# Performance work log

Measured on AMD Instinct MI355X. Metric: run time of the kernel, lower is better.

Reference implementation:

```python
import jax, jax.numpy as jnp
import numpy as np

D_MODEL = 1024
N_HEADS = 16
N_KV_HEADS = 4
HEAD_DIM = D_MODEL // N_HEADS
GROUP = N_HEADS // N_KV_HEADS
ROPE_BASE = 10000.0


def _rope(x):
    # x: (B, H, T, Dh); standard rotate-half RoPE, base 10000
    B, H, T, Dh = x.shape
    inv_freq = 1.0 / (ROPE_BASE ** (jnp.arange(0, Dh, 2, dtype=jnp.float32) / Dh))
    t = jnp.arange(T, dtype=jnp.float32)
    freqs = t[:, None] * inv_freq[None, :]              # (T, Dh/2)
    emb = jnp.concatenate([freqs, freqs], axis=-1)      # (T, Dh)
    cos = jnp.cos(emb)[None, None].astype(x.dtype)
    sin = jnp.sin(emb)[None, None].astype(x.dtype)
    x1, x2 = x[..., : Dh // 2], x[..., Dh // 2 :]
    rot = jnp.concatenate([-x2, x1], axis=-1)
    return x * cos + rot * sin


def setup_inputs() -> dict:
    key = jax.random.key(0)
    ks = jax.random.split(key, 5)
    B, T = 2, 2048
    s = 1.0 / np.sqrt(D_MODEL)
    return {
        "x": jax.random.normal(ks[0], (B, T, D_MODEL), dtype=jnp.float32),
        "wq": jax.random.normal(ks[1], (D_MODEL, N_HEADS * HEAD_DIM), dtype=jnp.float32) * s,
        "wk": jax.random.normal(ks[2], (D_MODEL, N_KV_HEADS * HEAD_DIM), dtype=jnp.float32) * s,
        "wv": jax.random.normal(ks[3], (D_MODEL, N_KV_HEADS * HEAD_DIM), dtype=jnp.float32) * s,
        "wo": jax.random.normal(ks[4], (N_HEADS * HEAD_DIM, D_MODEL), dtype=jnp.float32) * s,
    }


def reference(x, wq, wk, wv, wo):
    B, T, _ = x.shape
    q = (x @ wq).reshape(B, T, N_HEADS, HEAD_DIM).transpose(0, 2, 1, 3)      # (B,H,T,Dh)
    k = (x @ wk).reshape(B, T, N_KV_HEADS, HEAD_DIM).transpose(0, 2, 1, 3)   # (B,Hk,T,Dh)
    v = (x @ wv).reshape(B, T, N_KV_HEADS, HEAD_DIM).transpose(0, 2, 1, 3)
    q = _rope(q)
    k = _rope(k)
    # repeat_interleave kv heads group_size times -> (B, H, T, Dh)
    k = jnp.repeat(k, GROUP, axis=1)
    v = jnp.repeat(v, GROUP, axis=1)
    scale = 1.0 / np.sqrt(HEAD_DIM)
    scores = jnp.einsum("bhqd,bhkd->bhqk", q, k) * scale                      # (B,H,T,T)
    causal = jnp.tril(jnp.ones((T, T), dtype=bool))
    scores = jnp.where(causal[None, None], scores, -jnp.inf)
    attn = jax.nn.softmax(scores, axis=-1)
    out = jnp.einsum("bhqk,bhkd->bhqd", attn, v)                              # (B,H,T,Dh)
    out = out.transpose(0, 2, 1, 3).reshape(B, T, N_HEADS * HEAD_DIM)
    return out @ wo
```

## Files before the change

kernel.cpp:

```cpp
#include <hip/hip_runtime.h>

typedef short bshort8 __attribute__((ext_vector_type(8)));
typedef float f32x4 __attribute__((ext_vector_type(4)));

#define DEVFN static __device__ __forceinline__

DEVFN unsigned short f2bf(float f) {
    union { float f; unsigned u; } v; v.f = f;
    unsigned r = (v.u + 0x7FFFu + ((v.u >> 16) & 1u)) >> 16;
    return (unsigned short)r;
}

DEVFN float bf2f(unsigned short u) {
    union { unsigned u; float f; } v; v.u = (unsigned)u << 16;
    return v.f;
}

DEVFN unsigned cvt_pk_bf16(float a, float b) {
    unsigned r;
    asm("v_cvt_pk_bf16_f32 %0, %1, %2" : "=v"(r) : "v"(a), "v"(b));
    return r;
}

DEVFN float exp2_fast(float x) {
    float r;
    asm("v_exp_f32 %0, %1" : "=v"(r) : "v"(x));
    return r;
}

DEVFN float max3f(float a, float b, float c) {
    float r;
    asm("v_max3_f32 %0, %1, %2, %3" : "=v"(r) : "v"(a), "v"(b), "v"(c));
    return r;
}

DEVFN int swzf(int row) { return (row & 7) ^ ((row >> 3) & 7); }
DEVFN int swzf2(int row) { return (row & 3) ^ ((row >> 2) & 3); }

#define GLDS16(g, l)                                                            \
    __builtin_amdgcn_global_load_lds(                                           \
        (__attribute__((address_space(1))) void*)(g),                           \
        (__attribute__((address_space(3))) void*)(l), 16, 0, 0)

__global__ void prep_kernel(const float* __restrict__ x,
                            const float* __restrict__ wq,
                            const float* __restrict__ wk,
                            const float* __restrict__ wv,
                            const float* __restrict__ wo,
                            unsigned short* __restrict__ xb,
                            unsigned short* __restrict__ wt,
                            unsigned short* __restrict__ wot,
                            float2* __restrict__ cs) {
    const int z = blockIdx.z;
    int tx = threadIdx.x, ty = threadIdx.y;
    if (z >= 5) {
        int i = ((z - 5) * 1024 + blockIdx.y * 32 + blockIdx.x) * 256 + ty * 32 + tx;
        float4 v = ((const float4*)x)[i];
        ushort4 o;
        o.x = f2bf(v.x); o.y = f2bf(v.y); o.z = f2bf(v.z); o.w = f2bf(v.w);
        ((ushort4*)xb)[i] = o;
        return;
    }
    if (z == 4) {
        int idx = (blockIdx.y * 32 + blockIdx.x) * 256 + ty * 32 + tx;
        if (idx < 65536) {
            int t = idx >> 5, i = idx & 31;
            float inv_freq = powf(10000.0f, -(float)i / 32.0f);
            float a = (float)t * inv_freq;
            cs[idx] = make_float2(cosf(a), sinf(a));
        }
        return;
    }
    const float* src;
    unsigned short* dst;
    int N;
    if (z == 0)      { src = wq; dst = wt;                N = 1024; }
    else if (z == 1) { src = wk; dst = wt + 1024 * 1024;  N = 256; }
    else if (z == 2) { src = wv; dst = wt + 1280 * 1024;  N = 256; }
    else             { src = wo; dst = wot;               N = 1024; }
    if (blockIdx.x * 32 >= N) return;
    __shared__ float tile[32][33];
    int n0 = blockIdx.x * 32, k0 = blockIdx.y * 32;
#pragma unroll
    for (int i = 0; i < 4; i++)
        tile[ty + i * 8][tx] = src[(size_t)(k0 + ty + i * 8) * N + n0 + tx];
    __syncthreads();
#pragma unroll
    for (int i = 0; i < 4; i++)
        dst[(size_t)(n0 + ty + i * 8) * 1024 + k0 + tx] = f2bf(tile[tx][ty + i * 8]);
}


__global__ __launch_bounds__(256) void gemm_qkv_kernel(
    const unsigned short* __restrict__ xb, const unsigned short* __restrict__ wt,
    const float2* __restrict__ cs, unsigned short* __restrict__ Qb,
    unsigned short* __restrict__ Kb, unsigned short* __restrict__ Vt) {
    __shared__ char smem[49152];
    const int tid = threadIdx.x;
    const int lane = tid & 63, w = tid >> 6;
    const int m0 = blockIdx.y * 128, n0 = blockIdx.x * 64;
    const int l15 = lane & 15, g = lane >> 4;
    const int l8 = lane >> 3, c8 = lane & 7;

    const unsigned short* srcA[4];
    int dstA[4];
#pragma unroll
    for (int j = 0; j < 4; j++) {
        int row = w * 32 + j * 8 + l8;
        srcA[j] = xb + (size_t)(m0 + row) * 1024 + (c8 ^ swzf(row)) * 8;
        dstA[j] = w * 4096 + j * 1024 + lane * 16;
    }
    const unsigned short* srcB[2];
    int dstB[2];
#pragma unroll
    for (int j = 0; j < 2; j++) {
        int row = w * 16 + j * 8 + l8;
        srcB[j] = wt + (size_t)(n0 + row) * 1024 + (c8 ^ swzf(row)) * 8;
        dstB[j] = 0x8000 + w * 2048 + j * 1024 + lane * 16;
    }

    int aOff[2][2], bOff[4][2];
#pragma unroll
    for (int fm = 0; fm < 2; fm++) {
        int row = w * 32 + fm * 16 + l15;
#pragma unroll
        for (int ks = 0; ks < 2; ks++)
            aOff[fm][ks] = row * 128 + (((ks * 4 + g) ^ swzf(row)) << 4);
    }
#pragma unroll
    for (int fn = 0; fn < 4; fn++) {
        int row = fn * 16 + l15;
#pragma unroll
        for (int ks = 0; ks < 2; ks++)
            bOff[fn][ks] = row * 128 + (((ks * 4 + g) ^ swzf(row)) << 4);
    }

    f32x4 acc[2][4] = {};
#pragma unroll
    for (int j = 0; j < 4; j++) GLDS16(srcA[j], smem + dstA[j]);
#pragma unroll
    for (int j = 0; j < 2; j++) GLDS16(srcB[j], smem + dstB[j]);
    asm volatile("s_waitcnt vmcnt(0)" ::: "memory");
    __builtin_amdgcn_s_barrier();

    for (int kt = 0; kt < 16; kt++) {
        const int curA = (kt & 1) << 14;
        const int curB = (kt & 1) << 13;
        if (kt < 15) {
            const int nA = curA ^ 0x4000, nB = curB ^ 0x2000;
#pragma unroll
            for (int j = 0; j < 4; j++)
                GLDS16(srcA[j] + (kt + 1) * 64, smem + nA + dstA[j]);
#pragma unroll
            for (int j = 0; j < 2; j++)
                GLDS16(srcB[j] + (kt + 1) * 64, smem + nB + dstB[j]);
        }
        bshort8 af[2][2], bf[4][2];
#pragma unroll
        for (int fm = 0; fm < 2; fm++)
#pragma unroll
            for (int ks = 0; ks < 2; ks++)
                af[fm][ks] = *(const bshort8*)(smem + curA + aOff[fm][ks]);
#pragma unroll
        for (int fn = 0; fn < 4; fn++)
#pragma unroll
            for (int ks = 0; ks < 2; ks++)
                bf[fn][ks] = *(const bshort8*)(smem + 0x8000 + curB + bOff[fn][ks]);
        asm volatile("s_waitcnt lgkmcnt(0)" ::: "memory");
        __builtin_amdgcn_sched_barrier(0);
#pragma unroll
        for (int fm = 0; fm < 2; fm++)
#pragma unroll
            for (int fn = 0; fn < 4; fn++) {
                acc[fm][fn] = __builtin_amdgcn_mfma_f32_16x16x32_bf16(
                    af[fm][0], bf[fn][0], acc[fm][fn], 0, 0, 0);
                acc[fm][fn] = __builtin_amdgcn_mfma_f32_16x16x32_bf16(
                    af[fm][1], bf[fn][1], acc[fm][fn], 0, 0, 0);
            }
        if (kt < 15) {
            asm volatile("s_waitcnt vmcnt(0)" ::: "memory");
            __builtin_amdgcn_s_barrier();
        }
    }

    const bool isV = (n0 >= 1280);
    const bool isK = (n0 >= 1024) && !isV;
#pragma unroll
    for (int fm = 0; fm < 2; fm++) {
#pragma unroll
        for (int r = 0; r < 4; r++) {
            int m = m0 + w * 32 + fm * 16 + g * 4 + r;
            int b = m >> 11, t = m & 2047;
            if (isV) {
#pragma unroll
                for (int fn = 0; fn < 4; fn++) {
                    int n = n0 + fn * 16 + l15;
                    int d = n & 63, vh = (n - 1280) >> 6;
                    Vt[((size_t)(b * 4 + vh) * 64 + d) * 2048 + t] =
                        f2bf(acc[fm][fn][r]);
                }
            } else {
                float2 c0 = cs[t * 32 + l15];
                float2 c1 = cs[t * 32 + 16 + l15];
#pragma unroll
                for (int fn = 0; fn < 4; fn++) {
                    int n = n0 + fn * 16 + l15;
                    int d = n & 63;
                    float val = acc[fm][fn][r];
                    float pair = acc[fm][fn ^ 2][r];
                    float rot = (fn < 2) ? -pair : pair;
                    float2 cc = (fn & 1) ? c1 : c0;
                    float o = val * cc.x + rot * cc.y;
                    if (isK) {
                        int kh = (n - 1024) >> 6;
                        Kb[((size_t)(b * 4 + kh) * 2048 + t) * 64 + d] = f2bf(o);
                    } else {
                        o *= 0.1803368801111504f;
                        int h = n >> 6;
                        Qb[((size_t)(b * 16 + h) * 2048 + t) * 64 + d] = f2bf(o);
                    }
                }
            }
        }
    }
}


__global__ __launch_bounds__(256) void attn_kernel(
    const unsigned short* __restrict__ Qb, const unsigned short* __restrict__ Kb,
    const unsigned short* __restrict__ Vt, unsigned short* __restrict__ Opart,
    float* __restrict__ ml) {
    __shared__ char smem[40960];
    const int tid = threadIdx.x, lane = tid & 63, w = tid >> 6;
    const int l15 = lane & 15, g = lane >> 4;
    const int c = 79 - blockIdx.x;
    const int h = blockIdx.y, b = blockIdx.z;
    int qt, s;
    if (c < 8)       { qt = c;                    s = 0; }
    else if (c < 24) { qt = 8 + ((c - 8) >> 1);   s = (c - 8) & 1; }
    else if (c < 48) { qt = 16 + (c - 24) / 3;    s = (c - 24) % 3; }
    else             { qt = 24 + ((c - 48) >> 2); s = (c - 48) & 3; }
    const int k0t = s * 8;
    const int nk = min(8, qt + 1 - k0t);
    const int qs = qt * 64;
    const int kvh = h >> 2;
    const int slot = (b * 16 + h) * 80 + c;

    const unsigned short* Kbase = Kb + (size_t)(b * 4 + kvh) * 2048 * 64;
    const unsigned short* Vbase = Vt + (size_t)(b * 4 + kvh) * 64 * 2048;
    const unsigned short* Qhead = Qb + (size_t)(b * 16 + h) * 2048 * 64;

    const int srow8 = lane >> 3;
    const int sci = lane & 7;
    const int sk = (l15 & 7) ^ (l15 >> 3);
    const int strip = w * 2048;

    const int rowb = l15 * 128 + ((g ^ sk) << 4);
    const int Aq0 = strip + rowb;
    int Ak0 = 0x2000 + rowb;
    int Ak1 = Ak0 ^ 64;
    int Av0 = 0x6000 + rowb;
    int Av1 = Av0 ^ 64;
    const int pw0 = strip + l15 * 128 + (((2 * g) ^ sk) << 4);
    const int pw1 = strip + l15 * 128 + (((2 * g + 1) ^ sk) << 4);
    const int byteA0 = ((2 * g) & 3) * 32 + (g >> 1) * 8;
    const int byteB0 = ((2 * g + 1) & 3) * 32 + (g >> 1) * 8;
    const int prA0 = strip + l15 * 128 + (((byteA0 >> 4) ^ sk) << 4) + (byteA0 & 15);
    const int prB0 = strip + l15 * 128 + (((byteB0 >> 4) ^ sk) << 4) + (byteB0 & 15);

    const int lc0 = sci ^ srow8;
    const int lc1 = sci ^ srow8 ^ 1;
    const int r0 = w * 16 + srow8, r1 = w * 16 + 8 + srow8;

    GLDS16(Qhead + (size_t)(qs + r0) * 64 + lc0 * 8, smem + strip + lane * 16);
    GLDS16(Qhead + (size_t)(qs + r1) * 64 + lc1 * 8, smem + strip + lane * 16 + 1024);
    GLDS16(Kbase + (size_t)(k0t * 64 + r0) * 64 + lc0 * 8,
           smem + 0x2000 + strip + lane * 16);
    GLDS16(Kbase + (size_t)(k0t * 64 + r1) * 64 + lc1 * 8,
           smem + 0x2000 + strip + lane * 16 + 1024);
    GLDS16(Vbase + (size_t)r0 * 2048 + k0t * 64 + lc0 * 8,
           smem + 0x6000 + strip + lane * 16);
    GLDS16(Vbase + (size_t)r1 * 2048 + k0t * 64 + lc1 * 8,
           smem + 0x6000 + strip + lane * 16 + 1024);
    __syncthreads();

    bshort8 qf0 = *(const bshort8*)(smem + Aq0);
    bshort8 qf1 = *(const bshort8*)(smem + (Aq0 ^ 64));
    bshort8 ones;
#pragma unroll
    for (int j = 0; j < 8; j++) ones[j] = (short)0x3F80;

    const unsigned short* gk0 = Kbase + (size_t)((k0t + 1) * 64 + r0) * 64 + lc0 * 8;
    const unsigned short* gk1 = Kbase + (size_t)((k0t + 1) * 64 + r1) * 64 + lc1 * 8;
    const unsigned short* gv0 = Vbase + (size_t)r0 * 2048 + (k0t + 1) * 64 + lc0 * 8;
    const unsigned short* gv1 = Vbase + (size_t)r1 * 2048 + (k0t + 1) * 64 + lc1 * 8;
    int kdst = 0x4000 + strip + lane * 16;
    int vdst = 0x8000 + strip + lane * 16;

    float m_run = -1e30f;
    f32x4 l_acc = {};
    f32x4 O[4] = {};
    const int qlocal = w * 16 + l15;

    for (int kt = 0; kt < nk; kt++) {
        if (kt < nk - 1) {
            GLDS16(gk0, smem + kdst);
            GLDS16(gk1, smem + kdst + 1024);
            GLDS16(gv0, smem + vdst);
            GLDS16(gv1, smem + vdst + 1024);
            gk0 += 4096; gk1 += 4096; gv0 += 64; gv1 += 64;
        }
        f32x4 S[4];
        __builtin_amdgcn_s_setprio(1);
#pragma unroll
        for (int fn = 0; fn < 4; fn++) {
            bshort8 k0 = *(const bshort8*)(smem + Ak0 + fn * 2048);
            bshort8 k1 = *(const bshort8*)(smem + Ak1 + fn * 2048);
            f32x4 a = {};
            a = __builtin_amdgcn_mfma_f32_16x16x32_bf16(k0, qf0, a, 0, 0, 0);
            a = __builtin_amdgcn_mfma_f32_16x16x32_bf16(k1, qf1, a, 0, 0, 0);
            S[fn] = a;
        }
        __builtin_amdgcn_s_setprio(0);
        if (k0t + kt == qt) {
#pragma unroll
            for (int fn = 0; fn < 4; fn++)
#pragma unroll
                for (int r = 0; r < 4; r++)
                    if (fn * 16 + g * 4 + r > qlocal) S[fn][r] = -1e30f;
        }
        float ta = max3f(S[0][0], S[0][1], S[0][2]);
        float tb = max3f(S[0][3], S[1][0], S[1][1]);
        float tc = max3f(S[1][2], S[1][3], S[2][0]);
        float td = max3f(S[2][1], S[2][2], S[2][3]);
        float te = max3f(S[3][0], S[3][1], S[3][2]);
        float mt = fmaxf(max3f(ta, tb, tc), max3f(td, te, S[3][3]));
        mt = fmaxf(mt, __shfl_xor(mt, 16));
        mt = fmaxf(mt, __shfl_xor(mt, 32));
        if (!__all(mt <= m_run + 8.0f)) {
            float mn = fmaxf(m_run, mt);
            float alpha = exp2_fast(m_run - mn);
            m_run = mn;
            l_acc *= alpha;
#pragma unroll
            for (int fd = 0; fd < 4; fd++) O[fd] *= alpha;
        }
        float p[4][4];
#pragma unroll
        for (int fn = 0; fn < 4; fn++)
#pragma unroll
            for (int r = 0; r < 4; r++) p[fn][r] = exp2_fast(S[fn][r] - m_run);
        int4 w0v, w1v;
        w0v.x = cvt_pk_bf16(p[0][0], p[0][1]);
        w0v.y = cvt_pk_bf16(p[0][2], p[0][3]);
        w0v.z = cvt_pk_bf16(p[1][0], p[1][1]);
        w0v.w = cvt_pk_bf16(p[1][2], p[1][3]);
        w1v.x = cvt_pk_bf16(p[2][0], p[2][1]);
        w1v.y = cvt_pk_bf16(p[2][2], p[2][3]);
        w1v.z = cvt_pk_bf16(p[3][0], p[3][1]);
        w1v.w = cvt_pk_bf16(p[3][2], p[3][3]);
        *(int4*)(smem + pw0) = w0v;
        *(int4*)(smem + pw1) = w1v;
        asm volatile("s_waitcnt lgkmcnt(0)" ::: "memory");
        __builtin_amdgcn_sched_barrier(0);
        union PF { int2 d[2]; bshort8 v; };
        PF u0, u1;
        u0.d[0] = *(const int2*)(smem + prA0);
        u0.d[1] = *(const int2*)(smem + prB0);
        u1.d[0] = *(const int2*)(smem + (prA0 ^ 16));
        u1.d[1] = *(const int2*)(smem + (prB0 ^ 16));
        __builtin_amdgcn_s_setprio(1);
        l_acc = __builtin_amdgcn_mfma_f32_16x16x32_bf16(ones, u0.v, l_acc, 0, 0, 0);
        l_acc = __builtin_amdgcn_mfma_f32_16x16x32_bf16(ones, u1.v, l_acc, 0, 0, 0);
#pragma unroll
        for (int fd = 0; fd < 4; fd++) {
            bshort8 v0 = *(const bshort8*)(smem + Av0 + fd * 2048);
            bshort8 v1 = *(const bshort8*)(smem + Av1 + fd * 2048);
            O[fd] = __builtin_amdgcn_mfma_f32_16x16x32_bf16(v0, u0.v, O[fd], 0, 0, 0);
            O[fd] = __builtin_amdgcn_mfma_f32_16x16x32_bf16(v1, u1.v, O[fd], 0, 0, 0);
        }
        __builtin_amdgcn_s_setprio(0);
        Ak0 ^= 0x6000; Ak1 ^= 0x6000; Av0 ^= 0xE000; Av1 ^= 0xE000;
        kdst ^= 0x6000; vdst ^= 0xE000;
        if (kt < nk - 1) __syncthreads();
    }

    if (g == 0) {
        ((float2*)ml)[(size_t)slot * 64 + w * 16 + l15] =
            make_float2(m_run, l_acc[0]);
    }
#pragma unroll
    for (int fd = 0; fd < 4; fd++)
#pragma unroll
        for (int w2 = 0; w2 < 2; w2++) {
            unsigned word = cvt_pk_bf16(O[fd][2 * w2], O[fd][2 * w2 + 1]);
            int byte = fd * 32 + g * 8 + w2 * 4;
            *(unsigned*)(smem + strip + l15 * 128 + (((byte >> 4) ^ sk) << 4) +
                         (byte & 15)) = word;
        }
    asm volatile("s_waitcnt lgkmcnt(0)" ::: "memory");
    __builtin_amdgcn_sched_barrier(0);
#pragma unroll
    for (int it = 0; it < 2; it++) {
        int r16 = it * 8 + srow8;
        int4 vv = *(const int4*)(smem + strip + r16 * 128 +
                                 ((sci ^ srow8 ^ it) << 4));
        *(int4*)(Opart + (size_t)slot * 4096 + (w * 16 + r16) * 64 + sci * 8) = vv;
    }
}

__global__ __launch_bounds__(256) void combine_kernel(
    const unsigned short* __restrict__ Opart, const float* __restrict__ ml,
    unsigned short* __restrict__ Ob) {
    const int qt = blockIdx.x, h = blockIdx.y, b = blockIdx.z;
    const int S = (qt >> 3) + 1;
    int c0;
    if (qt < 8)       c0 = qt;
    else if (qt < 16) c0 = 8 + (qt - 8) * 2;
    else if (qt < 24) c0 = 24 + (qt - 16) * 3;
    else              c0 = 48 + (qt - 24) * 4;
    const int slotbase = (b * 16 + h) * 80 + c0;
    const int t = threadIdx.x;
    const int q = t >> 2, dq = (t & 3) * 16;
    const float2* ml2 = (const float2*)ml;

    float m[4], l[4];
    float mstar = -1e30f;
#pragma unroll
    for (int i = 0; i < 4; i++) {
        m[i] = -1e30f; l[i] = 0.f;
        if (i < S) {
            float2 v = ml2[(size_t)(slotbase + i) * 64 + q];
            m[i] = v.x; l[i] = v.y;
            mstar = fmaxf(mstar, v.x);
        }
    }
    float L = 0.f;
    float wgt[4];
#pragma unroll
    for (int i = 0; i < 4; i++) {
        wgt[i] = (i < S) ? exp2f(m[i] - mstar) : 0.f;
        L += wgt[i] * l[i];
    }
    float acc[16] = {};
#pragma unroll
    for (int i = 0; i < 4; i++) {
        if (i < S) {
            const unsigned short* P =
                Opart + (size_t)(slotbase + i) * 4096 + q * 64 + dq;
            int4 a0 = *(const int4*)P;
            int4 a1 = *(const int4*)(P + 8);
            unsigned u[8] = {(unsigned)a0.x, (unsigned)a0.y, (unsigned)a0.z,
                             (unsigned)a0.w, (unsigned)a1.x, (unsigned)a1.y,
                             (unsigned)a1.z, (unsigned)a1.w};
            float wi = wgt[i];
#pragma unroll
            for (int j = 0; j < 8; j++) {
                acc[2 * j]     += wi * bf2f((unsigned short)(u[j] & 0xFFFF));
                acc[2 * j + 1] += wi * bf2f((unsigned short)(u[j] >> 16));
            }
        }
    }
    float invL = 1.0f / L;
    int4 o0, o1;
    o0.x = cvt_pk_bf16(acc[0] * invL, acc[1] * invL);
    o0.y = cvt_pk_bf16(acc[2] * invL, acc[3] * invL);
    o0.z = cvt_pk_bf16(acc[4] * invL, acc[5] * invL);
    o0.w = cvt_pk_bf16(acc[6] * invL, acc[7] * invL);
    o1.x = cvt_pk_bf16(acc[8] * invL, acc[9] * invL);
    o1.y = cvt_pk_bf16(acc[10] * invL, acc[11] * invL);
    o1.z = cvt_pk_bf16(acc[12] * invL, acc[13] * invL);
    o1.w = cvt_pk_bf16(acc[14] * invL, acc[15] * invL);
    unsigned short* dst =
        Ob + (size_t)(b * 2048 + qt * 64 + q) * 1024 + h * 64 + dq;
    *(int4*)dst = o0;
    *(int4*)(dst + 8) = o1;
}

__global__ __launch_bounds__(256) void gemm_out_kernel(
    const unsigned short* __restrict__ ab, const unsigned short* __restrict__ wot,
    float* __restrict__ out) {
    __shared__ char smem[49152];
    const int tid = threadIdx.x;
    const int lane = tid & 63, w = tid >> 6;
    const int m0 = blockIdx.y * 128, n0 = blockIdx.x * 64;
    const int l15 = lane & 15, g = lane >> 4;
    const int l8 = lane >> 3, c8 = lane & 7;

    const unsigned short* srcA[4];
    int dstA[4];
#pragma unroll
    for (int j = 0; j < 4; j++) {
        int row = w * 32 + j * 8 + l8;
        srcA[j] = ab + (size_t)(m0 + row) * 1024 + (c8 ^ swzf(row)) * 8;
        dstA[j] = w * 4096 + j * 1024 + lane * 16;
    }
    const unsigned short* srcB[2];
    int dstB[2];
#pragma unroll
    for (int j = 0; j < 2; j++) {
        int row = w * 16 + j * 8 + l8;
        srcB[j] = wot + (size_t)(n0 + row) * 1024 + (c8 ^ swzf(row)) * 8;
        dstB[j] = 0x8000 + w * 2048 + j * 1024 + lane * 16;
    }

    int aOff[2][2], bOff[4][2];
#pragma unroll
    for (int fm = 0; fm < 2; fm++) {
        int row = w * 32 + fm * 16 + l15;
#pragma unroll
        for (int ks = 0; ks < 2; ks++)
            aOff[fm][ks] = row * 128 + (((ks * 4 + g) ^ swzf(row)) << 4);
    }
#pragma unroll
    for (int fn = 0; fn < 4; fn++) {
        int row = fn * 16 + l15;
#pragma unroll
        for (int ks = 0; ks < 2; ks++)
            bOff[fn][ks] = row * 128 + (((ks * 4 + g) ^ swzf(row)) << 4);
    }

    f32x4 acc[2][4] = {};
#pragma unroll
    for (int j = 0; j < 4; j++) GLDS16(srcA[j], smem + dstA[j]);
#pragma unroll
    for (int j = 0; j < 2; j++) GLDS16(srcB[j], smem + dstB[j]);
    asm volatile("s_waitcnt vmcnt(0)" ::: "memory");
    __builtin_amdgcn_s_barrier();

    for (int kt = 0; kt < 16; kt++) {
        const int curA = (kt & 1) << 14;
        const int curB = (kt & 1) << 13;
        if (kt < 15) {
            const int nA = curA ^ 0x4000, nB = curB ^ 0x2000;
#pragma unroll
            for (int j = 0; j < 4; j++)
                GLDS16(srcA[j] + (kt + 1) * 64, smem + nA + dstA[j]);
#pragma unroll
            for (int j = 0; j < 2; j++)
                GLDS16(srcB[j] + (kt + 1) * 64, smem + nB + dstB[j]);
        }
        bshort8 af[2][2], bf[4][2];
#pragma unroll
        for (int fm = 0; fm < 2; fm++)
#pragma unroll
            for (int ks = 0; ks < 2; ks++)
                af[fm][ks] = *(const bshort8*)(smem + curA + aOff[fm][ks]);
#pragma unroll
        for (int fn = 0; fn < 4; fn++)
#pragma unroll
            for (int ks = 0; ks < 2; ks++)
                bf[fn][ks] = *(const bshort8*)(smem + 0x8000 + curB + bOff[fn][ks]);
        asm volatile("s_waitcnt lgkmcnt(0)" ::: "memory");
        __builtin_amdgcn_sched_barrier(0);
#pragma unroll
        for (int fm = 0; fm < 2; fm++)
#pragma unroll
            for (int fn = 0; fn < 4; fn++) {
                acc[fm][fn] = __builtin_amdgcn_mfma_f32_16x16x32_bf16(
                    af[fm][0], bf[fn][0], acc[fm][fn], 0, 0, 0);
                acc[fm][fn] = __builtin_amdgcn_mfma_f32_16x16x32_bf16(
                    af[fm][1], bf[fn][1], acc[fm][fn], 0, 0, 0);
            }
        if (kt < 15) {
            asm volatile("s_waitcnt vmcnt(0)" ::: "memory");
            __builtin_amdgcn_s_barrier();
        }
    }
#pragma unroll
    for (int fm = 0; fm < 2; fm++)
#pragma unroll
        for (int r = 0; r < 4; r++) {
            int m = m0 + w * 32 + fm * 16 + g * 4 + r;
#pragma unroll
            for (int fn = 0; fn < 4; fn++) {
                int n = n0 + fn * 16 + l15;
                out[(size_t)m * 1024 + n] = acc[fm][fn][r];
            }
        }
}


extern "C" void kernel_launch(void* const* d_in, const int* in_sizes, int n_in,
                              void* d_out, int out_size, void* d_ws, size_t ws_size,
                              hipStream_t stream) {
    const float* x = (const float*)d_in[0];
    const float* wq = (const float*)d_in[1];
    const float* wk = (const float*)d_in[2];
    const float* wv = (const float*)d_in[3];
    const float* wo = (const float*)d_in[4];
    float* out = (float*)d_out;
    char* ws = (char*)d_ws;

    unsigned short* xb = (unsigned short*)(ws);
    unsigned short* wt = (unsigned short*)(ws + 8388608);
    float* ml = (float*)(ws + 8388608);
    unsigned short* wot = (unsigned short*)(ws + 11534336);
    float2* cs = (float2*)(ws + 13631488);
    unsigned short* Qb = (unsigned short*)(ws + 14155776);
    unsigned short* Kb = (unsigned short*)(ws + 22544384);
    unsigned short* Vtr = (unsigned short*)(ws + 26738688);
    unsigned short* Opart = (unsigned short*)(ws + 28835840);
    unsigned short* Ob = xb;

    hipLaunchKernelGGL(prep_kernel, dim3(32, 32, 9), dim3(32, 8), 0, stream, x,
                       wq, wk, wv, wo, xb, wt, wot, cs);
    hipLaunchKernelGGL(gemm_qkv_kernel, dim3(24, 32), dim3(256), 0, stream, xb, wt,
                       cs, Qb, Kb, Vtr);
    hipLaunchKernelGGL(attn_kernel, dim3(80, 16, 2), dim3(256), 0, stream, Qb, Kb,
                       Vtr, Opart, ml);
    hipLaunchKernelGGL(combine_kernel, dim3(32, 16, 2), dim3(256), 0, stream,
                       Opart, ml, Ob);
    hipLaunchKernelGGL(gemm_out_kernel, dim3(16, 32), dim3(256), 0, stream, Ob,
                       wot, out);
}
```

Baseline: 99.95 us.

## Single-buffer K tile and remap attention grid to group heads sharing KV

The attention kernel's K tile goes from double-buffered to single-buffered. The next K tile is loaded after an extra barrier that follows the QK^T MFMAs, while V stays double-buffered. This cuts shared memory from 40KB to 32KB, which could allow more resident blocks per CU. The grid is flattened to 1D and reordered so that consecutive blocks cover the 4 query heads of the same KV head and batch, which should improve L2 reuse of K/V. In exchange there is an extra barrier per iteration, and the K load latency is less hidden because it now overlaps only with the softmax and PV part of the step.

```diff
diff --git a/kernel.cpp b/kernel.cpp
--- a/kernel.cpp
+++ b/kernel.cpp
@@ -230,11 +230,16 @@
     const unsigned short* __restrict__ Qb, const unsigned short* __restrict__ Kb,
     const unsigned short* __restrict__ Vt, unsigned short* __restrict__ Opart,
     float* __restrict__ ml) {
-    __shared__ char smem[40960];
+    __shared__ char smem[32768];
     const int tid = threadIdx.x, lane = tid & 63, w = tid >> 6;
     const int l15 = lane & 15, g = lane >> 4;
-    const int c = 79 - blockIdx.x;
-    const int h = blockIdx.y, b = blockIdx.z;
+    const int id = blockIdx.x;
+    const int grp = id & 7;
+    const int b = grp >> 2, kvh = grp & 3;
+    const int i = id >> 3;
+    const int hh = i & 3;
+    const int h = kvh * 4 + hh;
+    const int c = 79 - (i >> 2);
     int qt, s;
     if (c < 8)       { qt = c;                    s = 0; }
     else if (c < 24) { qt = 8 + ((c - 8) >> 1);   s = (c - 8) & 1; }
@@ -243,7 +248,6 @@
     const int k0t = s * 8;
     const int nk = min(8, qt + 1 - k0t);
     const int qs = qt * 64;
-    const int kvh = h >> 2;
     const int slot = (b * 16 + h) * 80 + c;
 
     const unsigned short* Kbase = Kb + (size_t)(b * 4 + kvh) * 2048 * 64;
@@ -257,9 +261,9 @@
 
     const int rowb = l15 * 128 + ((g ^ sk) << 4);
     const int Aq0 = strip + rowb;
-    int Ak0 = 0x2000 + rowb;
-    int Ak1 = Ak0 ^ 64;
-    int Av0 = 0x6000 + rowb;
+    const int Ak0 = 0x2000 + rowb;
+    const int Ak1 = Ak0 ^ 64;
+    int Av0 = 0x4000 + rowb;
     int Av1 = Av0 ^ 64;
     const int pw0 = strip + l15 * 128 + (((2 * g) ^ sk) << 4);
     const int pw1 = strip + l15 * 128 + (((2 * g + 1) ^ sk) << 4);
@@ -271,17 +275,15 @@
     const int lc0 = sci ^ srow8;
     const int lc1 = sci ^ srow8 ^ 1;
     const int r0 = w * 16 + srow8, r1 = w * 16 + 8 + srow8;
+    const int kdst = 0x2000 + strip + lane * 16;
+    int vdst = 0x4000 + strip + lane * 16;
 
     GLDS16(Qhead + (size_t)(qs + r0) * 64 + lc0 * 8, smem + strip + lane * 16);
     GLDS16(Qhead + (size_t)(qs + r1) * 64 + lc1 * 8, smem + strip + lane * 16 + 1024);
-    GLDS16(Kbase + (size_t)(k0t * 64 + r0) * 64 + lc0 * 8,
-           smem + 0x2000 + strip + lane * 16);
-    GLDS16(Kbase + (size_t)(k0t * 64 + r1) * 64 + lc1 * 8,
-           smem + 0x2000 + strip + lane * 16 + 1024);
-    GLDS16(Vbase + (size_t)r0 * 2048 + k0t * 64 + lc0 * 8,
-           smem + 0x6000 + strip + lane * 16);
-    GLDS16(Vbase + (size_t)r1 * 2048 + k0t * 64 + lc1 * 8,
-           smem + 0x6000 + strip + lane * 16 + 1024);
+    GLDS16(Kbase + (size_t)(k0t * 64 + r0) * 64 + lc0 * 8, smem + kdst);
+    GLDS16(Kbase + (size_t)(k0t * 64 + r1) * 64 + lc1 * 8, smem + kdst + 1024);
+    GLDS16(Vbase + (size_t)r0 * 2048 + k0t * 64 + lc0 * 8, smem + vdst);
+    GLDS16(Vbase + (size_t)r1 * 2048 + k0t * 64 + lc1 * 8, smem + vdst + 1024);
     __syncthreads();
 
     bshort8 qf0 = *(const bshort8*)(smem + Aq0);
@@ -294,8 +296,6 @@
     const unsigned short* gk1 = Kbase + (size_t)((k0t + 1) * 64 + r1) * 64 + lc1 * 8;
     const unsigned short* gv0 = Vbase + (size_t)r0 * 2048 + (k0t + 1) * 64 + lc0 * 8;
     const unsigned short* gv1 = Vbase + (size_t)r1 * 2048 + (k0t + 1) * 64 + lc1 * 8;
-    int kdst = 0x4000 + strip + lane * 16;
-    int vdst = 0x8000 + strip + lane * 16;
 
     float m_run = -1e30f;
     f32x4 l_acc = {};
@@ -304,11 +304,9 @@
 
     for (int kt = 0; kt < nk; kt++) {
         if (kt < nk - 1) {
-            GLDS16(gk0, smem + kdst);
-            GLDS16(gk1, smem + kdst + 1024);
-            GLDS16(gv0, smem + vdst);
-            GLDS16(gv1, smem + vdst + 1024);
-            gk0 += 4096; gk1 += 4096; gv0 += 64; gv1 += 64;
+            GLDS16(gv0, smem + (vdst ^ 0x2000));
+            GLDS16(gv1, smem + (vdst ^ 0x2000) + 1024);
+            gv0 += 64; gv1 += 64;
         }
         f32x4 S[4];
         __builtin_amdgcn_s_setprio(1);
@@ -322,6 +320,12 @@
             S[fn] = a;
         }
         __builtin_amdgcn_s_setprio(0);
+        __builtin_amdgcn_s_barrier();
+        if (kt < nk - 1) {
+            GLDS16(gk0, smem + kdst);
+            GLDS16(gk1, smem + kdst + 1024);
+            gk0 += 4096; gk1 += 4096;
+        }
         if (k0t + kt == qt) {
 #pragma unroll
             for (int fn = 0; fn < 4; fn++)
@@ -380,8 +384,7 @@
             O[fd] = __builtin_amdgcn_mfma_f32_16x16x32_bf16(v1, u1.v, O[fd], 0, 0, 0);
         }
         __builtin_amdgcn_s_setprio(0);
-        Ak0 ^= 0x6000; Ak1 ^= 0x6000; Av0 ^= 0xE000; Av1 ^= 0xE000;
-        kdst ^= 0x6000; vdst ^= 0xE000;
+        Av0 ^= 0x2000; Av1 ^= 0x2000; vdst ^= 0x2000;
         if (kt < nk - 1) __syncthreads();
     }
 
@@ -607,7 +610,7 @@
                        wq, wk, wv, wo, xb, wt, wot, cs);
     hipLaunchKernelGGL(gemm_qkv_kernel, dim3(24, 32), dim3(256), 0, stream, xb, wt,
                        cs, Qb, Kb, Vtr);
-    hipLaunchKernelGGL(attn_kernel, dim3(80, 16, 2), dim3(256), 0, stream, Qb, Kb,
+    hipLaunchKernelGGL(attn_kernel, dim3(2560), dim3(256), 0, stream, Qb, Kb,
                        Vtr, Opart, ml);
     hipLaunchKernelGGL(combine_kernel, dim3(32, 16, 2), dim3(256), 0, stream,
                        Opart, ml, Ob);
```

Result: faster. 97.85 us (-2.1%).
